# Kernel tuning notes

Measured on AMD Instinct MI355X. Metric: run time of the kernel, lower is better.

The kernel has to match this reference:

```python
import math
import jax, jax.numpy as jnp
import numpy as np

B_SZ = 32768   # batch (reflections)
S = 4          # mc_samples
D_IN = 256     # encoder dim
LAT = 8        # latent dim
NBINS = 300    # resolution x angle bins
K = 1323       # profile pixels
R = 4          # CP rank


def setup_inputs() -> dict:
    key = jax.random.key(0)
    ks = jax.random.split(key, 8)
    x = jax.random.normal(ks[0], (B_SZ, D_IN), jnp.float32)
    group_labels = jax.random.randint(ks[1], (B_SZ,), 0, NBINS)
    eps = jax.random.normal(ks[2], (S, B_SZ, LAT), jnp.float32)  # reparam noise
    A = jax.random.normal(ks[3], (NBINS, R), jnp.float32) * 0.01
    B = jax.random.normal(ks[4], (K, R), jnp.float32) * 0.01
    C = jax.random.normal(ks[5], (LAT, R), jnp.float32) * 0.01
    b = jnp.zeros((NBINS, K), jnp.float32)
    # nn.Linear default init (kaiming-uniform approx via small normal is fine for a numeric baseline)
    bound = 1.0 / math.sqrt(D_IN)
    mu_w = jax.random.uniform(ks[6], (LAT, D_IN), jnp.float32, -bound, bound)
    mu_b = jax.random.uniform(ks[7], (LAT,), jnp.float32, -bound, bound)
    std_w = jnp.zeros((LAT, D_IN), jnp.float32)  # nn.init.zeros_
    std_b = jnp.full((LAT,), math.log(math.exp(0.5) - 1.0), jnp.float32)  # softplus^-1(0.5)
    return dict(x=x, eps=eps, A=A, B=B, C=C, b=b, mu_w=mu_w, mu_b=mu_b,
                std_w=std_w, std_b=std_b, group_labels=group_labels)


def reference(x, eps, A, B, C, b, mu_w, mu_b, std_w, std_b, group_labels):
    mu_h = x @ mu_w.T + mu_b                      # (B, d)
    std_h = jax.nn.softplus(x @ std_w.T + std_b)  # (B, d)
    h = mu_h + std_h * eps                        # rsample: (S, B, d)

    A_n = A[group_labels]                         # (B, R)  per-bin gather
    b_n = b[group_labels]                         # (B, K)  per-bin gather

    z = h @ C                                     # (S, B, R)
    logits = (A_n * z) @ B.T + b_n                # (S, B, K)
    zp = jax.nn.softmax(logits, axis=-1)

    z_mean = mu_h @ C                             # (B, R)
    mean_logits = (A_n * z_mean) @ B.T + b_n      # (B, K)
    mean_profile = jax.nn.softmax(mean_logits, axis=-1)
    return zp, mean_profile, mu_h, std_h
```

## Files before the change

### kernel.cpp

```cpp
#include <hip/hip_runtime.h>

#define B_SZ  32768
#define S_MC  4
#define D_IN  256
#define LAT   8
#define NBINS 300
#define KDIM  1323
#define RNK   4

constexpr int TPB   = 256;
constexpr int KPT   = (KDIM + TPB - 1) / TPB;
constexpr int BPB   = 4;
constexpr int NPASS = S_MC + 1;

__global__ __launch_bounds__(TPB) void cp_profile_kernel(
    const float* __restrict__ x,
    const float* __restrict__ eps,
    const float* __restrict__ A,
    const float* __restrict__ Bm,
    const float* __restrict__ C,
    const float* __restrict__ bias,
    const float* __restrict__ mu_w,
    const float* __restrict__ mu_b,
    const float* __restrict__ std_w,
    const float* __restrict__ std_b,
    const int*   __restrict__ glab,
    float* __restrict__ out)
{
    __shared__ float muh_s[LAT];
    __shared__ float stdh_s[LAT];
    __shared__ float w_s[NPASS][RNK];
    __shared__ float redmax_s[4][NPASS];
    __shared__ float redsum_s[4][NPASS];

    const int tid  = threadIdx.x;
    const int lane = tid & 63;
    const int wid  = tid >> 6;

    float4 b4[KPT];
    const float4* B4 = reinterpret_cast<const float4*>(Bm);
    #pragma unroll
    for (int i = 0; i < KPT; ++i) {
        const int k = tid + i * TPB;
        b4[i] = (k < KDIM) ? B4[k] : make_float4(0.f, 0.f, 0.f, 0.f);
    }

    for (int bb = 0; bb < BPB; ++bb) {
        const int b = blockIdx.x * BPB + bb;
        const int g = glab[b];

        float bn[KPT];
        #pragma unroll
        for (int i = 0; i < KPT; ++i) {
            const int k = tid + i * TPB;
            bn[i] = (k < KDIM) ? bias[(size_t)g * KDIM + k] : 0.f;
        }

        const float4* x4 = reinterpret_cast<const float4*>(x + (size_t)b * D_IN);
        const float4 xv = x4[lane];
        float dotv[4];
        #pragma unroll
        for (int dd = 0; dd < 4; ++dd) {
            const int d = wid * 4 + dd;
            const float4* W4 = reinterpret_cast<const float4*>(
                (d < LAT) ? (mu_w + d * D_IN) : (std_w + (d - LAT) * D_IN));
            const float4 wv = W4[lane];
            float a = xv.x * wv.x + xv.y * wv.y + xv.z * wv.z + xv.w * wv.w;
            #pragma unroll
            for (int off = 32; off > 0; off >>= 1)
                a += __shfl_xor(a, off, 64);
            dotv[dd] = a;
        }
        if (lane == 0) {
            #pragma unroll
            for (int dd = 0; dd < 4; ++dd) {
                const int d = wid * 4 + dd;
                if (d < LAT) {
                    muh_s[d] = dotv[dd] + mu_b[d];
                } else {
                    const float y = dotv[dd] + std_b[d - LAT];
                    stdh_s[d - LAT] = fmaxf(y, 0.f) + log1pf(expf(-fabsf(y)));
                }
            }
        }
        __syncthreads();

        if (tid < 20) {
            const int s = tid >> 2, r = tid & 3;
            const float* ep = eps + ((size_t)(s < S_MC ? s : 0) * B_SZ + b) * LAT;
            float z = 0.f;
            #pragma unroll
            for (int j = 0; j < LAT; ++j) {
                float h = muh_s[j];
                if (s < S_MC) h += stdh_s[j] * ep[j];
                z += h * C[j * RNK + r];
            }
            w_s[s][r] = A[g * RNK + r] * z;
        }
        const size_t base_small = (size_t)NPASS * B_SZ * KDIM;
        if (tid >= 32 && tid < 40)
            out[base_small + (size_t)b * LAT + (tid - 32)] = muh_s[tid - 32];
        if (tid >= 40 && tid < 48)
            out[base_small + (size_t)B_SZ * LAT + (size_t)b * LAT + (tid - 40)] = stdh_s[tid - 40];
        __syncthreads();

        float wr[NPASS][RNK];
        #pragma unroll
        for (int s = 0; s < NPASS; ++s)
            #pragma unroll
            for (int r = 0; r < RNK; ++r)
                wr[s][r] = w_s[s][r];

        float lmax[NPASS];
        #pragma unroll
        for (int s = 0; s < NPASS; ++s) lmax[s] = -INFINITY;
        #pragma unroll
        for (int i = 0; i < KPT; ++i) {
            const int    k  = tid + i * TPB;
            const bool   ok = (k < KDIM);
            const float4 bv = b4[i];
            const float  bi = bn[i];
            #pragma unroll
            for (int s = 0; s < NPASS; ++s) {
                float v = fmaf(wr[s][0], bv.x,
                          fmaf(wr[s][1], bv.y,
                          fmaf(wr[s][2], bv.z, wr[s][3] * bv.w))) + bi;
                lmax[s] = fmaxf(lmax[s], ok ? v : -INFINITY);
            }
        }
        #pragma unroll
        for (int s = 0; s < NPASS; ++s)
            #pragma unroll
            for (int off = 32; off > 0; off >>= 1)
                lmax[s] = fmaxf(lmax[s], __shfl_xor(lmax[s], off, 64));
        if (lane == 0) {
            #pragma unroll
            for (int s = 0; s < NPASS; ++s) redmax_s[wid][s] = lmax[s];
        }
        __syncthreads();

        float m[NPASS];
        #pragma unroll
        for (int s = 0; s < NPASS; ++s)
            m[s] = fmaxf(fmaxf(redmax_s[0][s], redmax_s[1][s]),
                         fmaxf(redmax_s[2][s], redmax_s[3][s]));

        float lsum[NPASS];
        #pragma unroll
        for (int s = 0; s < NPASS; ++s) lsum[s] = 0.f;
        #pragma unroll
        for (int i = 0; i < KPT; ++i) {
            const int    k  = tid + i * TPB;
            const bool   ok = (k < KDIM);
            const float4 bv = b4[i];
            const float  bi = bn[i];
            #pragma unroll
            for (int s = 0; s < NPASS; ++s) {
                const float v = fmaf(wr[s][0], bv.x,
                               fmaf(wr[s][1], bv.y,
                               fmaf(wr[s][2], bv.z, wr[s][3] * bv.w))) + bi;
                lsum[s] += ok ? __expf(v - m[s]) : 0.f;
            }
        }
        #pragma unroll
        for (int s = 0; s < NPASS; ++s)
            #pragma unroll
            for (int off = 32; off > 0; off >>= 1)
                lsum[s] += __shfl_xor(lsum[s], off, 64);
        if (lane == 0) {
            #pragma unroll
            for (int s = 0; s < NPASS; ++s) redsum_s[wid][s] = lsum[s];
        }
        __syncthreads();

        float inv[NPASS];
        #pragma unroll
        for (int s = 0; s < NPASS; ++s)
            inv[s] = 1.f / (redsum_s[0][s] + redsum_s[1][s] +
                            redsum_s[2][s] + redsum_s[3][s]);

        #pragma unroll
        for (int i = 0; i < KPT; ++i) {
            const int    k  = tid + i * TPB;
            const bool   ok = (k < KDIM);
            const float4 bv = b4[i];
            const float  bi = bn[i];
            #pragma unroll
            for (int s = 0; s < NPASS; ++s) {
                const float v = fmaf(wr[s][0], bv.x,
                               fmaf(wr[s][1], bv.y,
                               fmaf(wr[s][2], bv.z, wr[s][3] * bv.w))) + bi;
                if (ok) {
                    const size_t obase = (s < S_MC)
                        ? ((size_t)((size_t)s * B_SZ + b) * KDIM)
                        : ((size_t)S_MC * B_SZ * KDIM + (size_t)b * KDIM);
                    __builtin_nontemporal_store(__expf(v - m[s]) * inv[s],
                                                &out[obase + k]);
                }
            }
        }
    }
}

extern "C" void kernel_launch(void* const* d_in, const int* in_sizes, int n_in,
                              void* d_out, int out_size, void* d_ws, size_t ws_size,
                              hipStream_t stream) {
    const float* x     = (const float*)d_in[0];
    const float* eps   = (const float*)d_in[1];
    const float* A     = (const float*)d_in[2];
    const float* Bm    = (const float*)d_in[3];
    const float* C     = (const float*)d_in[4];
    const float* bias  = (const float*)d_in[5];
    const float* mu_w  = (const float*)d_in[6];
    const float* mu_b  = (const float*)d_in[7];
    const float* std_w = (const float*)d_in[8];
    const float* std_b = (const float*)d_in[9];
    const int*   glab  = (const int*)d_in[10];
    float* out = (float*)d_out;

    cp_profile_kernel<<<B_SZ / BPB, TPB, 0, stream>>>(
        x, eps, A, Bm, C, bias, mu_w, mu_b, std_w, std_b, glab, out);
}
```

Baseline: 1.077 ms.

## Vectorize profile stores to 16-byte aligned float4 chunks per row

Each row's K=1323 outputs are remapped so every thread owns contiguous groups of four pixels, aligned using the row's offset modulo 4. The softmax outputs can then be written as 16-byte nontemporal vector stores, with a few scalar stores for the unaligned head and tail. Rows of B and the bias are now reloaded per reflection instead of caching B in registers once per block. This raises per-row load traffic and adds index complexity in exchange for wider, fewer store instructions on a store-bound kernel.

Measured after the change: 1.109 ms. +3.0%, slower.

```diff
diff --git a/kernel.cpp b/kernel.cpp
--- a/kernel.cpp
+++ b/kernel.cpp
@@ -8,10 +8,14 @@
 #define KDIM  1323
 #define RNK   4
 
+typedef float f32x4 __attribute__((ext_vector_type(4)));
+
 constexpr int TPB   = 256;
-constexpr int KPT   = (KDIM + TPB - 1) / TPB;
 constexpr int BPB   = 4;
 constexpr int NPASS = S_MC + 1;
+constexpr int NF4   = 330;
+constexpr int ITER1 = NF4 - TPB;
+
 
 __global__ __launch_bounds__(TPB) void cp_profile_kernel(
     const float* __restrict__ x,
@@ -36,35 +40,22 @@
     const int tid  = threadIdx.x;
     const int lane = tid & 63;
     const int wid  = tid >> 6;
-
-    float4 b4[KPT];
-    const float4* B4 = reinterpret_cast<const float4*>(Bm);
-    #pragma unroll
-    for (int i = 0; i < KPT; ++i) {
-        const int k = tid + i * TPB;
-        b4[i] = (k < KDIM) ? B4[k] : make_float4(0.f, 0.f, 0.f, 0.f);
-    }
+    const f32x4* B4 = reinterpret_cast<const f32x4*>(Bm);
 
     for (int bb = 0; bb < BPB; ++bb) {
         const int b = blockIdx.x * BPB + bb;
         const int g = glab[b];
-
-        float bn[KPT];
-        #pragma unroll
-        for (int i = 0; i < KPT; ++i) {
-            const int k = tid + i * TPB;
-            bn[i] = (k < KDIM) ? bias[(size_t)g * KDIM + k] : 0.f;
-        }
-
-        const float4* x4 = reinterpret_cast<const float4*>(x + (size_t)b * D_IN);
-        const float4 xv = x4[lane];
+        const int p = b & 3;
+
+        const f32x4* x4 = reinterpret_cast<const f32x4*>(x + (size_t)b * D_IN);
+        const f32x4 xv = x4[lane];
         float dotv[4];
         #pragma unroll
         for (int dd = 0; dd < 4; ++dd) {
             const int d = wid * 4 + dd;
-            const float4* W4 = reinterpret_cast<const float4*>(
+            const f32x4* W4 = reinterpret_cast<const f32x4*>(
                 (d < LAT) ? (mu_w + d * D_IN) : (std_w + (d - LAT) * D_IN));
-            const float4 wv = W4[lane];
+            const f32x4 wv = W4[lane];
             float a = xv.x * wv.x + xv.y * wv.y + xv.z * wv.z + xv.w * wv.w;
             #pragma unroll
             for (int off = 32; off > 0; off >>= 1)
@@ -111,22 +102,43 @@
             for (int r = 0; r < RNK; ++r)
                 wr[s][r] = w_s[s][r];
 
+        const int  k0 = p + 4 * tid;
+        const bool v1 = (tid < ITER1);
+        const int  k1 = p + 4 * (TPB + tid);
+        const int  e  = tid - 100;
+        const bool vht = (e >= 0 && e < 3);
+        const int  kht = vht ? ((e < p) ? e : (1320 + e)) : 0;
+
+        const float* biasg = bias + (size_t)g * KDIM;
+        f32x4 br0[4], br1[4];
+        float bv0[4], bv1[4];
+        #pragma unroll
+        for (int q = 0; q < 4; ++q) {
+            br0[q] = B4[k0 + q];
+            bv0[q] = biasg[k0 + q];
+            if (v1) { br1[q] = B4[k1 + q]; bv1[q] = biasg[k1 + q]; }
+            else    { br1[q] = (f32x4)(0.f); bv1[q] = -INFINITY; }
+        }
+        f32x4 brht = (f32x4)(0.f);
+        float bvht = -INFINITY;
+        if (vht) { brht = B4[kht]; bvht = biasg[kht]; }
+
+        auto LG = [&](const f32x4& r4, float bi, int s) -> float {
+            return fmaf(wr[s][0], r4.x,
+                   fmaf(wr[s][1], r4.y,
+                   fmaf(wr[s][2], r4.z, wr[s][3] * r4.w))) + bi;
+        };
+
         float lmax[NPASS];
         #pragma unroll
-        for (int s = 0; s < NPASS; ++s) lmax[s] = -INFINITY;
-        #pragma unroll
-        for (int i = 0; i < KPT; ++i) {
-            const int    k  = tid + i * TPB;
-            const bool   ok = (k < KDIM);
-            const float4 bv = b4[i];
-            const float  bi = bn[i];
-            #pragma unroll
-            for (int s = 0; s < NPASS; ++s) {
-                float v = fmaf(wr[s][0], bv.x,
-                          fmaf(wr[s][1], bv.y,
-                          fmaf(wr[s][2], bv.z, wr[s][3] * bv.w))) + bi;
-                lmax[s] = fmaxf(lmax[s], ok ? v : -INFINITY);
-            }
+        for (int s = 0; s < NPASS; ++s) {
+            float m0 = -INFINITY;
+            #pragma unroll
+            for (int q = 0; q < 4; ++q) {
+                m0 = fmaxf(m0, LG(br0[q], bv0[q], s));
+                m0 = fmaxf(m0, LG(br1[q], bv1[q], s));
+            }
+            lmax[s] = fmaxf(m0, LG(brht, bvht, s));
         }
         #pragma unroll
         for (int s = 0; s < NPASS; ++s)
@@ -147,20 +159,14 @@
 
         float lsum[NPASS];
         #pragma unroll
-        for (int s = 0; s < NPASS; ++s) lsum[s] = 0.f;
-        #pragma unroll
-        for (int i = 0; i < KPT; ++i) {
-            const int    k  = tid + i * TPB;
-            const bool   ok = (k < KDIM);
-            const float4 bv = b4[i];
-            const float  bi = bn[i];
-            #pragma unroll
-            for (int s = 0; s < NPASS; ++s) {
-                const float v = fmaf(wr[s][0], bv.x,
-                               fmaf(wr[s][1], bv.y,
-                               fmaf(wr[s][2], bv.z, wr[s][3] * bv.w))) + bi;
-                lsum[s] += ok ? __expf(v - m[s]) : 0.f;
-            }
+        for (int s = 0; s < NPASS; ++s) {
+            float a = 0.f;
+            #pragma unroll
+            for (int q = 0; q < 4; ++q) {
+                a += __expf(LG(br0[q], bv0[q], s) - m[s]);
+                a += __expf(LG(br1[q], bv1[q], s) - m[s]);
+            }
+            lsum[s] = a + __expf(LG(brht, bvht, s) - m[s]);
         }
         #pragma unroll
         for (int s = 0; s < NPASS; ++s)
@@ -180,23 +186,29 @@
                             redsum_s[2][s] + redsum_s[3][s]);
 
         #pragma unroll
-        for (int i = 0; i < KPT; ++i) {
-            const int    k  = tid + i * TPB;
-            const bool   ok = (k < KDIM);
-            const float4 bv = b4[i];
-            const float  bi = bn[i];
-            #pragma unroll
-            for (int s = 0; s < NPASS; ++s) {
-                const float v = fmaf(wr[s][0], bv.x,
-                               fmaf(wr[s][1], bv.y,
-                               fmaf(wr[s][2], bv.z, wr[s][3] * bv.w))) + bi;
-                if (ok) {
-                    const size_t obase = (s < S_MC)
-                        ? ((size_t)((size_t)s * B_SZ + b) * KDIM)
-                        : ((size_t)S_MC * B_SZ * KDIM + (size_t)b * KDIM);
-                    __builtin_nontemporal_store(__expf(v - m[s]) * inv[s],
-                                                &out[obase + k]);
-                }
+        for (int s = 0; s < NPASS; ++s) {
+            const size_t ob = (s < S_MC)
+                ? ((size_t)((size_t)s * B_SZ + b) * KDIM)
+                : ((size_t)S_MC * B_SZ * KDIM + (size_t)b * KDIM);
+            f32x4 o0;
+            o0.x = __expf(LG(br0[0], bv0[0], s) - m[s]) * inv[s];
+            o0.y = __expf(LG(br0[1], bv0[1], s) - m[s]) * inv[s];
+            o0.z = __expf(LG(br0[2], bv0[2], s) - m[s]) * inv[s];
+            o0.w = __expf(LG(br0[3], bv0[3], s) - m[s]) * inv[s];
+            __builtin_nontemporal_store(
+                o0, reinterpret_cast<f32x4*>(out + ob + k0));
+            if (v1) {
+                f32x4 o1;
+                o1.x = __expf(LG(br1[0], bv1[0], s) - m[s]) * inv[s];
+                o1.y = __expf(LG(br1[1], bv1[1], s) - m[s]) * inv[s];
+                o1.z = __expf(LG(br1[2], bv1[2], s) - m[s]) * inv[s];
+                o1.w = __expf(LG(br1[3], bv1[3], s) - m[s]) * inv[s];
+                __builtin_nontemporal_store(
+                    o1, reinterpret_cast<f32x4*>(out + ob + k1));
+            }
+            if (vht) {
+                const float v = __expf(LG(brht, bvht, s) - m[s]) * inv[s];
+                __builtin_nontemporal_store(v, out + ob + kht);
             }
         }
     }
```
